# Kernel tuning notes

Hardware: AMD Instinct MI355X
Metric: run time of the kernel (lower is better)

The kernel has to match this reference:

```python
import jax, jax.numpy as jnp
import numpy as np

N, E, D, L = 50000, 800000, 128, 4


def setup_inputs() -> dict:
    key = jax.random.key(0)
    k0, k1, k2, k3 = jax.random.split(key, 4)
    x = jax.random.normal(k0, (N, D), dtype=jnp.float32)
    edge_index = jax.random.randint(k1, (2, E), 0, N, dtype=jnp.int32)
    # per-layer GCNConv weights [L, D, D] and biases [L, D]
    W = jax.random.normal(k2, (L, D, D), dtype=jnp.float32) * (1.0 / np.sqrt(D))
    b = jax.random.normal(k3, (L, D), dtype=jnp.float32) * 0.01
    batch_index = jnp.zeros((N,), dtype=jnp.int32)
    node_rankings = jnp.zeros((N,), dtype=jnp.int32)
    return {"x": x, "edge_index": edge_index, "batch_index": batch_index,
            "node_rankings": node_rankings, "W": W, "b": b}


def reference(x, edge_index, batch_index, node_rankings, W, b):
    # NullControl contributes 0; dropout_rate=0 / eval -> identity.
    n = x.shape[0]
    loops = jnp.arange(n, dtype=edge_index.dtype)
    row = jnp.concatenate([edge_index[0], loops])  # sources (with self-loops)
    col = jnp.concatenate([edge_index[1], loops])  # destinations
    # symmetric GCN normalization: deg over destinations, norm = d_i^-1/2 d_j^-1/2
    deg = jax.ops.segment_sum(jnp.ones_like(row, dtype=x.dtype), col, num_segments=n)
    dinv = jnp.where(deg > 0, jax.lax.rsqrt(deg), 0.0)
    norm = dinv[row] * dinv[col]  # [E+N]
    for l in range(W.shape[0]):
        h = x @ W[l]                      # [N, D] dense transform
        msg = h[row] * norm[:, None]      # [E+N, D] gathered, scaled messages
        agg = jax.ops.segment_sum(msg, col, num_segments=n)  # scatter-add
        x = jax.nn.relu(agg + b[l])       # control(=0) + bias + relu
    return x
```

## Files before the change

### kernel.cpp

```cpp
#include <hip/hip_runtime.h>

#define D 128
#define NLAYERS 4

typedef unsigned short ushort_t;
typedef unsigned int uint_t;
typedef __attribute__((ext_vector_type(8))) short short8;
typedef __attribute__((ext_vector_type(4))) float f32x4;

__device__ __forceinline__ ushort_t f2bf(float f) {
    uint_t u = __float_as_uint(f);
    u += 0x7FFFu + ((u >> 16) & 1u);
    return (ushort_t)(u >> 16);
}
__device__ __forceinline__ float bf_lo(uint_t u) {
    return __uint_as_float(u << 16);
}
__device__ __forceinline__ float bf_hi(uint_t u) {
    return __uint_as_float(u & 0xFFFF0000u);
}
__device__ __forceinline__ uint_t pack2(float a, float b) {
    return (uint_t)f2bf(a) | ((uint_t)f2bf(b) << 16);
}


__global__ void k_count_deg(const int* __restrict__ dsts, int E,
                            int* __restrict__ deg, int* __restrict__ slot) {
    int i = blockIdx.x * blockDim.x + threadIdx.x;
    if (i < E) slot[i] = atomicAdd(&deg[dsts[i]], 1);
}

__global__ void k_scan1(const int* __restrict__ deg, int n, int* __restrict__ prow,
                        int* __restrict__ partials, float* __restrict__ dinv) {
    __shared__ int wsum[4];
    int tid = threadIdx.x;
    int base = blockIdx.x * 1024 + tid * 4;
    int g0 = (base + 0 < n) ? deg[base + 0] : -4;
    int g1 = (base + 1 < n) ? deg[base + 1] : -4;
    int g2 = (base + 2 < n) ? deg[base + 2] : -4;
    int g3 = (base + 3 < n) ? deg[base + 3] : -4;
    if (base + 0 < n) dinv[base + 0] = rsqrtf((float)(g0 + 1));
    if (base + 1 < n) dinv[base + 1] = rsqrtf((float)(g1 + 1));
    if (base + 2 < n) dinv[base + 2] = rsqrtf((float)(g2 + 1));
    if (base + 3 < n) dinv[base + 3] = rsqrtf((float)(g3 + 1));
    int p0 = (g0 + 4) & ~3;
    int p1 = (g1 + 4) & ~3;
    int p2 = (g2 + 4) & ~3;
    int p3 = (g3 + 4) & ~3;
    int s = p0 + p1 + p2 + p3;
    int lane = tid & 63;
    int incl = s;
    #pragma unroll
    for (int off = 1; off < 64; off <<= 1) {
        int y = __shfl_up(incl, off);
        if (lane >= off) incl += y;
    }
    int wid = tid >> 6;
    if (lane == 63) wsum[wid] = incl;
    __syncthreads();
    int wprev = 0;
    for (int w = 0; w < wid; w++) wprev += wsum[w];
    int excl = wprev + (incl - s);
    if (base + 0 < n) prow[base + 0] = excl;
    if (base + 1 < n) prow[base + 1] = excl + p0;
    if (base + 2 < n) prow[base + 2] = excl + p0 + p1;
    if (base + 3 < n) prow[base + 3] = excl + p0 + p1 + p2;
    if (tid == 255) partials[blockIdx.x] = wprev + incl;
}

__global__ void k_scan23(int* __restrict__ prow, const int* __restrict__ partials,
                         int n, int nb) {
    int i = blockIdx.x * blockDim.x + threadIdx.x;
    int chunk = (blockIdx.x * blockDim.x) >> 10;
    int pre = 0;
    for (int j = 0; j < chunk; j++) pre += partials[j];
    if (i < n) prow[i] += pre;
    if (i == 0) {
        int tot = 0;
        for (int j = 0; j < nb; j++) tot += partials[j];
        prow[n] = tot;
    }
}

__global__ void k_prep(const int* __restrict__ srcs, const int* __restrict__ dsts,
                       const int* __restrict__ deg, const int* __restrict__ slot,
                       const int* __restrict__ prow, const float* __restrict__ dinv,
                       const float* __restrict__ x, const float* __restrict__ W,
                       int* __restrict__ ewi, ushort_t* __restrict__ xs0,
                       ushort_t* __restrict__ xs1, ushort_t* __restrict__ Wt_hi,
                       ushort_t* __restrict__ Wt_lo, int n, int E,
                       int B1, int B2, int B3, int B4) {
    int b = blockIdx.x;
    int tid = threadIdx.x;
    if (b < B1) {
        int i = b * 256 + tid;
        if (i < E) {
            int c = dsts[i];
            ewi[prow[c] + 1 + slot[i]] = srcs[i];
        }
    } else if (b < B2) {
        int i = (b - B1) * 256 + tid;
        if (i < n) {
            int base = prow[i];
            int len = deg[i] + 1;
            int plen = (deg[i] + 4) & ~3;
            ewi[base] = i;
            for (int j = len; j < plen; j++) ewi[base + j] = n;
        }
    } else if (b < B3) {
        int idx = (b - B2) * 256 + tid;
        if (idx < n * (D / 4)) {
            int row = idx >> 5;
            float di = dinv[row];
            float4 v = ((const float4*)x)[idx];
            uint2 o;
            o.x = pack2(di * v.x, di * v.y);
            o.y = pack2(di * v.z, di * v.w);
            ((uint2*)xs0)[idx] = o;
        }
    } else if (b < B4) {
        int t = (b - B3) * 256 + tid;
        int l = t >> 14;
        int k = (t >> 7) & 127;
        int nn = t & 127;
        float w = W[((size_t)l << 14) + k * 128 + nn];
        ushort_t hi = f2bf(w);
        float wf = __uint_as_float((uint_t)hi << 16);
        ushort_t lo = f2bf(w - wf);
        size_t o = ((size_t)l << 14) + nn * 128 + k;
        Wt_hi[o] = hi;
        Wt_lo[o] = lo;
    } else {
        if (tid < 128) xs0[(size_t)n * D + tid] = 0;
        else xs1[(size_t)n * D + (tid - 128)] = 0;
    }
}

__global__ __launch_bounds__(256) void k_aggregate(
    const ushort_t* __restrict__ xs, const int* __restrict__ prow,
    const int* __restrict__ ewi, const float* __restrict__ dinv,
    ushort_t* __restrict__ s, int n) {
    int gwave = (blockIdx.x * 256 + threadIdx.x) >> 6;
    if (gwave >= n) return;
    int lane = threadIdx.x & 63;
    int sub = lane >> 4;
    int t = lane & 15;
    int node = gwave;
    float di = dinv[node];

    float acc[8] = {0.f, 0.f, 0.f, 0.f, 0.f, 0.f, 0.f, 0.f};
    int e = prow[node], end = prow[node + 1];
    for (; e + 16 <= end; e += 16) {
        int4 gg = *(const int4*)(ewi + e + sub * 4);
        uint4 v0 = *(const uint4*)(xs + (size_t)gg.x * D + t * 8);
        uint4 v1 = *(const uint4*)(xs + (size_t)gg.y * D + t * 8);
        uint4 v2 = *(const uint4*)(xs + (size_t)gg.z * D + t * 8);
        uint4 v3 = *(const uint4*)(xs + (size_t)gg.w * D + t * 8);
        acc[0] += bf_lo(v0.x); acc[1] += bf_hi(v0.x);
        acc[2] += bf_lo(v0.y); acc[3] += bf_hi(v0.y);
        acc[4] += bf_lo(v0.z); acc[5] += bf_hi(v0.z);
        acc[6] += bf_lo(v0.w); acc[7] += bf_hi(v0.w);
        acc[0] += bf_lo(v1.x); acc[1] += bf_hi(v1.x);
        acc[2] += bf_lo(v1.y); acc[3] += bf_hi(v1.y);
        acc[4] += bf_lo(v1.z); acc[5] += bf_hi(v1.z);
        acc[6] += bf_lo(v1.w); acc[7] += bf_hi(v1.w);
        acc[0] += bf_lo(v2.x); acc[1] += bf_hi(v2.x);
        acc[2] += bf_lo(v2.y); acc[3] += bf_hi(v2.y);
        acc[4] += bf_lo(v2.z); acc[5] += bf_hi(v2.z);
        acc[6] += bf_lo(v2.w); acc[7] += bf_hi(v2.w);
        acc[0] += bf_lo(v3.x); acc[1] += bf_hi(v3.x);
        acc[2] += bf_lo(v3.y); acc[3] += bf_hi(v3.y);
        acc[4] += bf_lo(v3.z); acc[5] += bf_hi(v3.z);
        acc[6] += bf_lo(v3.w); acc[7] += bf_hi(v3.w);
    }
    for (; e < end; e += 4) {
        int g = ewi[e + sub];
        uint4 v = *(const uint4*)(xs + (size_t)g * D + t * 8);
        acc[0] += bf_lo(v.x); acc[1] += bf_hi(v.x);
        acc[2] += bf_lo(v.y); acc[3] += bf_hi(v.y);
        acc[4] += bf_lo(v.z); acc[5] += bf_hi(v.z);
        acc[6] += bf_lo(v.w); acc[7] += bf_hi(v.w);
    }
    #pragma unroll
    for (int q = 0; q < 8; q++) {
        acc[q] += __shfl_xor(acc[q], 16);
        acc[q] += __shfl_xor(acc[q], 32);
    }
    if (sub == 0) {
        ushort_t* dst = s + (size_t)node * D + t * 8;
        uint4 o;
        o.x = pack2(di * acc[0], di * acc[1]);
        o.y = pack2(di * acc[2], di * acc[3]);
        o.z = pack2(di * acc[4], di * acc[5]);
        o.w = pack2(di * acc[6], di * acc[7]);
        *(uint4*)dst = o;
    }
}

__global__ __launch_bounds__(256) void k_gemm_mfma(
    const ushort_t* __restrict__ A, const ushort_t* __restrict__ Wt_hi,
    const ushort_t* __restrict__ Wt_lo, const float* __restrict__ bias,
    const float* __restrict__ dinv, float* __restrict__ out_f32,
    ushort_t* __restrict__ out_bf, int n) {
    int tid = threadIdx.x;
    int wave = tid >> 6;
    int lane = tid & 63;
    int lg = lane >> 4;
    int lr = lane & 15;
    int base_row = blockIdx.x * 128 + wave * 32;

    short8 a[2][4];
    #pragma unroll
    for (int st = 0; st < 2; st++) {
        int r = base_row + st * 16 + lr;
        if (r > n - 1) r = n - 1;
        const ushort_t* ap = A + (size_t)r * D + lg * 8;
        #pragma unroll
        for (int k0 = 0; k0 < 4; k0++)
            a[st][k0] = *(const short8*)(ap + k0 * 32);
    }

    f32x4 acc[2][8];
    #pragma unroll
    for (int st = 0; st < 2; st++)
        #pragma unroll
        for (int nt = 0; nt < 8; nt++)
            acc[st][nt] = (f32x4){0.f, 0.f, 0.f, 0.f};

    #pragma unroll
    for (int nt = 0; nt < 8; nt++) {
        const ushort_t* wh = Wt_hi + (size_t)(nt * 16 + lr) * D + lg * 8;
        const ushort_t* wl = Wt_lo + (size_t)(nt * 16 + lr) * D + lg * 8;
        #pragma unroll
        for (int k0 = 0; k0 < 4; k0++) {
            short8 bh = *(const short8*)(wh + k0 * 32);
            short8 bl = *(const short8*)(wl + k0 * 32);
            acc[0][nt] = __builtin_amdgcn_mfma_f32_16x16x32_bf16(a[0][k0], bh, acc[0][nt], 0, 0, 0);
            acc[0][nt] = __builtin_amdgcn_mfma_f32_16x16x32_bf16(a[0][k0], bl, acc[0][nt], 0, 0, 0);
            acc[1][nt] = __builtin_amdgcn_mfma_f32_16x16x32_bf16(a[1][k0], bh, acc[1][nt], 0, 0, 0);
            acc[1][nt] = __builtin_amdgcn_mfma_f32_16x16x32_bf16(a[1][k0], bl, acc[1][nt], 0, 0, 0);
        }
    }

    #pragma unroll
    for (int nt = 0; nt < 8; nt++) {
        int col = nt * 16 + lr;
        float bv = bias[col];
        #pragma unroll
        for (int st = 0; st < 2; st++) {
            #pragma unroll
            for (int r = 0; r < 4; r++) {
                int grow = base_row + st * 16 + lg * 4 + r;
                if (grow < n) {
                    float o = fmaxf(acc[st][nt][r] + bv, 0.f);
                    if (out_bf) out_bf[(size_t)grow * D + col] = f2bf(dinv[grow] * o);
                    else out_f32[(size_t)grow * D + col] = o;
                }
            }
        }
    }
}


extern "C" void kernel_launch(void* const* d_in, const int* in_sizes, int n_in,
                              void* d_out, int out_size, void* d_ws, size_t ws_size,
                              hipStream_t stream) {
    const float* x   = (const float*)d_in[0];
    const int* eidx  = (const int*)d_in[1];
    const float* W   = (const float*)d_in[4];
    const float* b   = (const float*)d_in[5];
    float* out       = (float*)d_out;

    const int N = in_sizes[0] / D;
    const int E = in_sizes[1] / 2;
    const int* srcs = eidx;
    const int* dsts = eidx + E;

    char* ws = (char*)d_ws;
    size_t off = 0;
    auto alloc = [&](size_t bytes) -> void* {
        void* p = ws + off;
        off = (off + bytes + 511) & ~(size_t)511;
        return p;
    };
    int*      deg      = (int*)alloc((size_t)N * 4);
    float*    dinv     = (float*)alloc((size_t)N * 4);
    int*      prow     = (int*)alloc((size_t)(N + 1) * 4);
    int*      partials = (int*)alloc(256 * 4);
    int*      ewi      = (int*)alloc((size_t)(E + 4 * N) * 4);
    ushort_t* s_buf    = (ushort_t*)alloc((size_t)N * D * 2);
    ushort_t* xh0      = (ushort_t*)alloc(((size_t)N + 1) * D * 2);
    ushort_t* xh1      = (ushort_t*)alloc(((size_t)N + 1) * D * 2);
    ushort_t* wt_hi    = (ushort_t*)alloc((size_t)NLAYERS * D * D * 2);
    ushort_t* wt_lo    = (ushort_t*)alloc((size_t)NLAYERS * D * D * 2);
    int*      slot     = (int*)s_buf;
    (void)ws_size; (void)n_in; (void)out_size;

    hipMemsetAsync(deg, 0, (size_t)N * 4, stream);

    int tE = (E + 255) / 256;
    int tN = (N + 255) / 256;
    int nbScan = (N + 1023) / 1024;

    k_count_deg<<<tE, 256, 0, stream>>>(dsts, E, deg, slot);
    k_scan1<<<nbScan, 256, 0, stream>>>(deg, N, prow, partials, dinv);
    k_scan23<<<tN, 256, 0, stream>>>(prow, partials, N, nbScan);

    int B1 = tE;
    int B2 = B1 + tN;
    int B3 = B2 + (N * (D / 4) + 255) / 256;
    int B4 = B3 + (NLAYERS * D * D) / 256;
    k_prep<<<B4 + 1, 256, 0, stream>>>(srcs, dsts, deg, slot, prow, dinv, x, W,
                                       ewi, xh0, xh1, wt_hi, wt_lo, N, E,
                                       B1, B2, B3, B4);

    int aggBlocks = (N + 3) / 4;
    int gemmBlocks = (N + 127) / 128;

    const ushort_t* xin = xh0;
    for (int l = 0; l < NLAYERS; l++) {
        k_aggregate<<<aggBlocks, 256, 0, stream>>>(xin, prow, ewi, dinv, s_buf, N);
        bool last = (l == NLAYERS - 1);
        ushort_t* xout = last ? nullptr : ((l & 1) ? xh0 : xh1);
        k_gemm_mfma<<<gemmBlocks, 256, 0, stream>>>(
            s_buf, wt_hi + (size_t)l * D * D, wt_lo + (size_t)l * D * D,
            b + (size_t)l * D, dinv, last ? out : nullptr, xout, N);
        xin = xout;
    }
}
```

Before: 390.8 us.

## Use half-wave per node in aggregation with 8-padded CSR, pack GEMM stores

The aggregation kernel now gives each node 32 lanes (two 16-lane groups) instead of a full 64-lane wave, so twice as many nodes run per block. CSR rows are padded to a multiple of 8 so the 4-wide unrolled gather loop needs no tail loop, at the cost of more dummy gathers from the zero row. The GEMM epilogue exchanges neighbouring columns with a shuffle and writes packed pairs, halving the number of store instructions. With an average degree around 17, the per-node padding overhead rises, and each node's edge loads are spread over fewer lanes.

```diff
diff --git a/kernel.cpp b/kernel.cpp
--- a/kernel.cpp
+++ b/kernel.cpp
@@ -35,18 +35,18 @@
     __shared__ int wsum[4];
     int tid = threadIdx.x;
     int base = blockIdx.x * 1024 + tid * 4;
-    int g0 = (base + 0 < n) ? deg[base + 0] : -4;
-    int g1 = (base + 1 < n) ? deg[base + 1] : -4;
-    int g2 = (base + 2 < n) ? deg[base + 2] : -4;
-    int g3 = (base + 3 < n) ? deg[base + 3] : -4;
+    int g0 = (base + 0 < n) ? deg[base + 0] : -8;
+    int g1 = (base + 1 < n) ? deg[base + 1] : -8;
+    int g2 = (base + 2 < n) ? deg[base + 2] : -8;
+    int g3 = (base + 3 < n) ? deg[base + 3] : -8;
     if (base + 0 < n) dinv[base + 0] = rsqrtf((float)(g0 + 1));
     if (base + 1 < n) dinv[base + 1] = rsqrtf((float)(g1 + 1));
     if (base + 2 < n) dinv[base + 2] = rsqrtf((float)(g2 + 1));
     if (base + 3 < n) dinv[base + 3] = rsqrtf((float)(g3 + 1));
-    int p0 = (g0 + 4) & ~3;
-    int p1 = (g1 + 4) & ~3;
-    int p2 = (g2 + 4) & ~3;
-    int p3 = (g3 + 4) & ~3;
+    int p0 = (g0 + 8) & ~7;
+    int p1 = (g1 + 8) & ~7;
+    int p2 = (g2 + 8) & ~7;
+    int p3 = (g3 + 8) & ~7;
     int s = p0 + p1 + p2 + p3;
     int lane = tid & 63;
     int incl = s;
@@ -103,7 +103,7 @@
         if (i < n) {
             int base = prow[i];
             int len = deg[i] + 1;
-            int plen = (deg[i] + 4) & ~3;
+            int plen = (deg[i] + 8) & ~7;
             ewi[base] = i;
             for (int j = len; j < plen; j++) ewi[base + j] = n;
         }
@@ -140,17 +140,16 @@
     const ushort_t* __restrict__ xs, const int* __restrict__ prow,
     const int* __restrict__ ewi, const float* __restrict__ dinv,
     ushort_t* __restrict__ s, int n) {
-    int gwave = (blockIdx.x * 256 + threadIdx.x) >> 6;
-    if (gwave >= n) return;
+    int node = (blockIdx.x * 256 + threadIdx.x) >> 5;
+    if (node >= n) return;
     int lane = threadIdx.x & 63;
-    int sub = lane >> 4;
+    int sub = (lane >> 4) & 1;
     int t = lane & 15;
-    int node = gwave;
     float di = dinv[node];
 
     float acc[8] = {0.f, 0.f, 0.f, 0.f, 0.f, 0.f, 0.f, 0.f};
     int e = prow[node], end = prow[node + 1];
-    for (; e + 16 <= end; e += 16) {
+    for (; e < end; e += 8) {
         int4 gg = *(const int4*)(ewi + e + sub * 4);
         uint4 v0 = *(const uint4*)(xs + (size_t)gg.x * D + t * 8);
         uint4 v1 = *(const uint4*)(xs + (size_t)gg.y * D + t * 8);
@@ -173,19 +172,8 @@
         acc[4] += bf_lo(v3.z); acc[5] += bf_hi(v3.z);
         acc[6] += bf_lo(v3.w); acc[7] += bf_hi(v3.w);
     }
-    for (; e < end; e += 4) {
-        int g = ewi[e + sub];
-        uint4 v = *(const uint4*)(xs + (size_t)g * D + t * 8);
-        acc[0] += bf_lo(v.x); acc[1] += bf_hi(v.x);
-        acc[2] += bf_lo(v.y); acc[3] += bf_hi(v.y);
-        acc[4] += bf_lo(v.z); acc[5] += bf_hi(v.z);
-        acc[6] += bf_lo(v.w); acc[7] += bf_hi(v.w);
-    }
-    #pragma unroll
-    for (int q = 0; q < 8; q++) {
-        acc[q] += __shfl_xor(acc[q], 16);
-        acc[q] += __shfl_xor(acc[q], 32);
-    }
+    #pragma unroll
+    for (int q = 0; q < 8; q++) acc[q] += __shfl_xor(acc[q], 16);
     if (sub == 0) {
         ushort_t* dst = s + (size_t)node * D + t * 8;
         uint4 o;
@@ -251,10 +239,16 @@
             #pragma unroll
             for (int r = 0; r < 4; r++) {
                 int grow = base_row + st * 16 + lg * 4 + r;
-                if (grow < n) {
-                    float o = fmaxf(acc[st][nt][r] + bv, 0.f);
-                    if (out_bf) out_bf[(size_t)grow * D + col] = f2bf(dinv[grow] * o);
-                    else out_f32[(size_t)grow * D + col] = o;
+                float o = fmaxf(acc[st][nt][r] + bv, 0.f);
+                float op = __shfl_xor(o, 1);
+                if ((lr & 1) == 0 && grow < n) {
+                    if (out_bf) {
+                        float dsc = dinv[grow];
+                        *(uint_t*)(out_bf + (size_t)grow * D + col) = pack2(dsc * o, dsc * op);
+                    } else {
+                        float2 ov; ov.x = o; ov.y = op;
+                        *(float2*)(out_f32 + (size_t)grow * D + col) = ov;
+                    }
                 }
             }
         }
@@ -287,7 +281,7 @@
     float*    dinv     = (float*)alloc((size_t)N * 4);
     int*      prow     = (int*)alloc((size_t)(N + 1) * 4);
     int*      partials = (int*)alloc(256 * 4);
-    int*      ewi      = (int*)alloc((size_t)(E + 4 * N) * 4);
+    int*      ewi      = (int*)alloc((size_t)(E + 8 * N) * 4);
     ushort_t* s_buf    = (ushort_t*)alloc((size_t)N * D * 2);
     ushort_t* xh0      = (ushort_t*)alloc(((size_t)N + 1) * D * 2);
     ushort_t* xh1      = (ushort_t*)alloc(((size_t)N + 1) * D * 2);
@@ -314,7 +308,7 @@
                                        ewi, xh0, xh1, wt_hi, wt_lo, N, E,
                                        B1, B2, B3, B4);
 
-    int aggBlocks = (N + 3) / 4;
+    int aggBlocks = (N + 7) / 8;
     int gemmBlocks = (N + 127) / 128;
 
     const ushort_t* xin = xh0;
```

After: 372.8 us. -4.6%, faster.
